# Performance work log

Hardware: AMD Instinct MI355X
Metric: run time of the kernel (lower is better)

The kernel has to match this reference:

```python
import jax, jax.numpy as jnp
import numpy as np

DIM = 128          # per-stream channels (init arg `dim`)
C = 2 * DIM        # fused channels
NH = 8             # num_heads
HD = C // NH       # head_dim = 32
K = 3              # kernel_size
DIL = (2, 3)       # dilation list
ND = len(DIL)
SCALE = HD ** -0.5


def setup_inputs() -> dict:
    key = jax.random.key(0)
    ks = jax.random.split(key, 4)
    B, H, W = 4, 80, 80
    rgb = jax.random.normal(ks[0], (B, DIM, H, W), jnp.float32)
    ir = jax.random.normal(ks[1], (B, DIM, H, W), jnp.float32)
    w_qkv = jax.random.normal(ks[2], (3 * C, C), jnp.float32) * (C ** -0.5)
    w_proj = jax.random.normal(ks[3], (C, C), jnp.float32) * (C ** -0.5)
    b_proj = jnp.zeros((C,), jnp.float32)
    return {"rgb": rgb, "ir": ir, "w_qkv": w_qkv, "w_proj": w_proj, "b_proj": b_proj}


def _unfold(x, k, d):
    # nn.Unfold(k, dilation=d, padding=d*(k-1)//2, stride=1) -> [B, c, k*k, H, W]
    B, c, H, W = x.shape
    p = d * (k - 1) // 2
    xp = jnp.pad(x, ((0, 0), (0, 0), (p, p), (p, p)))
    pats = [xp[:, :, i * d:i * d + H, j * d:j * d + W]
            for i in range(k) for j in range(k)]
    return jnp.stack(pats, axis=2)


def _dilate_attention(q, k, v, d):
    # q,k,v: [B, c, H, W] with c = C // ND; attention over k*k dilated neighborhood
    B, c, H, W = q.shape
    h = c // HD
    N = H * W
    qr = q.reshape(B, h, HD, N)                      # [B,h,hd,N]
    ku = _unfold(k, K, d).reshape(B, h, HD, K * K, N)  # [B,h,hd,K2,N]
    vu = _unfold(v, K, d).reshape(B, h, HD, K * K, N)
    attn = jnp.einsum('bhdn,bhdkn->bhnk', qr, ku) * SCALE   # [B,h,N,K2]
    attn = jax.nn.softmax(attn, axis=-1)
    out = jnp.einsum('bhnk,bhdkn->bnhd', attn, vu)          # head-major channels
    return out.reshape(B, H, W, c)


def reference(rgb, ir, w_qkv, w_proj, b_proj):
    y = jnp.concatenate([rgb, ir], axis=1)            # [B, C, H, W]
    B, Cc, H, W = y.shape
    # 1x1 conv qkv, then split channels as [3, num_dilation, C//num_dilation]
    qkv = jnp.einsum('bchw,oc->bohw', y, w_qkv).reshape(B, 3, ND, Cc // ND, H, W)
    outs = [_dilate_attention(qkv[:, 0, i], qkv[:, 1, i], qkv[:, 2, i], DIL[i])
            for i in range(ND)]
    x = jnp.concatenate(outs, axis=-1)                # [B, H, W, C], dilation-major
    x = x @ w_proj.T + b_proj                         # proj Linear(C, C)
    # residual: add rgb to first half of channels, ir to second half
    return x + y.transpose(0, 2, 3, 1)
```

## Files before the change

### kernel.cpp

```cpp
#include <hip/hip_runtime.h>

#define HH 80
#define WW 80
#define NPIX 6400
#define NB 4
#define BN 25600
#define CDIM 256
#define QKVC 768
#define SCALE 0.17677669529663689f

typedef __attribute__((ext_vector_type(8))) short short8;
typedef __attribute__((ext_vector_type(4))) float floatx4;

__device__ __forceinline__ float b2f(ushort u) {
    return __uint_as_float(((uint)u) << 16);
}
__device__ __forceinline__ ushort f2b(float f) {
    uint u = __float_as_uint(f);
    return (ushort)((u + 0x7fffu + ((u >> 16) & 1u)) >> 16);
}
__device__ __forceinline__ void unpack8(uint4 v, float* f) {
    f[0] = __uint_as_float(v.x << 16); f[1] = __uint_as_float(v.x & 0xffff0000u);
    f[2] = __uint_as_float(v.y << 16); f[3] = __uint_as_float(v.y & 0xffff0000u);
    f[4] = __uint_as_float(v.z << 16); f[5] = __uint_as_float(v.z & 0xffff0000u);
    f[6] = __uint_as_float(v.w << 16); f[7] = __uint_as_float(v.w & 0xffff0000u);
}
__device__ __forceinline__ void gload_lds16(const void* gptr, void* lptr) {
    __builtin_amdgcn_global_load_lds(
        (const __attribute__((address_space(1))) unsigned int*)gptr,
        (__attribute__((address_space(3))) unsigned int*)lptr,
        16, 0, 0);
}

__global__ __launch_bounds__(256) void cast_all_k(
    const float* __restrict__ rgb, const float* __restrict__ ir,
    const float* __restrict__ wq, const float* __restrict__ wp,
    ushort* __restrict__ Yb, ushort* __restrict__ wqb, ushort* __restrict__ wpb)
{
    const int tid = threadIdx.x;
    if (blockIdx.x >= 100) {
        int i = (((blockIdx.x - 100) * 8 + blockIdx.y) * 4 + blockIdx.z) * 256 + tid;
        if (i < QKVC * CDIM) wqb[i] = f2b(wq[i]);
        else                 wpb[i - QKVC * CDIM] = f2b(wp[i - QKVC * CDIM]);
        return;
    }
    __shared__ ushort T[32][72];
    const int pix0 = blockIdx.x * 64;
    const int cb = blockIdx.y;
    const int b = blockIdx.z;

    const int pl = tid & 63, cg = tid >> 6;
    #pragma unroll
    for (int cc = 0; cc < 32; cc += 4) {
        int c = cb * 32 + cc + cg;
        const float* src = (c < 128) ? (rgb + ((size_t)b * 128 + c) * NPIX)
                                     : (ir + ((size_t)b * 128 + (c - 128)) * NPIX);
        T[cc + cg][pl] = f2b(src[pix0 + pl]);
    }
    __syncthreads();
    const int nl = tid >> 2, c0 = (tid & 3) * 8;
    ushort tmp[8];
    #pragma unroll
    for (int j = 0; j < 8; ++j) tmp[j] = T[c0 + j][nl];
    uint4 v;
    v.x = tmp[0] | ((uint)tmp[1] << 16);
    v.y = tmp[2] | ((uint)tmp[3] << 16);
    v.z = tmp[4] | ((uint)tmp[5] << 16);
    v.w = tmp[6] | ((uint)tmp[7] << 16);
    *(uint4*)(&Yb[((size_t)(b * NPIX + pix0 + nl)) * CDIM + cb * 32 + c0]) = v;
}

__device__ __forceinline__ void gemm_nt_body64(
    const ushort* __restrict__ A, const ushort* __restrict__ W,
    ushort* As, ushort* Bs, int n0, int o0, floatx4 acc[4][4])
{
    const int tid = threadIdx.x;
    const int lane = tid & 63;
    const int wave = tid >> 6;
    const int wr = wave >> 1, wc = wave & 1;
    const int l15 = lane & 15, quad = lane >> 4;

    const int srow8 = tid >> 3;
    const int scol  = ((tid & 7) * 8) ^ ((srow8 & 1) << 5);
    const int par   = l15 & 1;

    for (int k0 = 0; k0 < CDIM; k0 += 64) {
        #pragma unroll
        for (int r = 0; r < 4; ++r) {
            const int row = r * 32 + srow8;
            gload_lds16(&A[(size_t)(n0 + row) * CDIM + k0 + scol],
                        As + r * 2048 + wave * 512);
            gload_lds16(&W[(size_t)(o0 + row) * CDIM + k0 + scol],
                        Bs + r * 2048 + wave * 512);
        }
        __syncthreads();
        #pragma unroll
        for (int s = 0; s < 2; ++s) {
            const int fc = ((s ^ par) << 5) + quad * 8;
            short8 af[4], bfr[4];
            #pragma unroll
            for (int i = 0; i < 4; ++i)
                af[i] = *(const short8*)(&As[(wr * 64 + i * 16 + l15) * 64 + fc]);
            #pragma unroll
            for (int j = 0; j < 4; ++j)
                bfr[j] = *(const short8*)(&Bs[(wc * 64 + j * 16 + l15) * 64 + fc]);
            #pragma unroll
            for (int i = 0; i < 4; ++i)
                #pragma unroll
                for (int j = 0; j < 4; ++j)
                    acc[i][j] = __builtin_amdgcn_mfma_f32_16x16x32_bf16(
                        bfr[j], af[i], acc[i][j], 0, 0, 0);
        }
        __syncthreads();
    }
}

__global__ __launch_bounds__(256) void gemm_qkv_mfma(
    const ushort* __restrict__ Yb, const ushort* __restrict__ Wb,
    ushort* __restrict__ qkv2)
{
    __shared__ __align__(16) ushort As[128 * 64];
    __shared__ __align__(16) ushort Bs[128 * 64];
    const int tid = threadIdx.x;
    const int lane = tid & 63;
    const int wave = tid >> 6;
    const int wr = wave >> 1, wc = wave & 1;
    const int l15 = lane & 15, quad = lane >> 4;

    const int bid = blockIdx.x;
    const int swz = (bid & 7) * 150 + (bid >> 3);
    const int n0 = (swz / 6) * 128;
    const int o0 = (swz % 6) * 128;

    floatx4 acc[4][4] = {};
    gemm_nt_body64(Yb, Wb, As, Bs, n0, o0, acc);

    #pragma unroll
    for (int i = 0; i < 4; ++i) {
        const int n = n0 + wr * 64 + i * 16 + l15;
        #pragma unroll
        for (int j = 0; j < 4; ++j) {
            const int o4 = o0 + wc * 64 + j * 16 + quad * 4;
            uint2 v;
            v.x = f2b(acc[i][j][0]) | ((uint)f2b(acc[i][j][1]) << 16);
            v.y = f2b(acc[i][j][2]) | ((uint)f2b(acc[i][j][3]) << 16);
            *(uint2*)(qkv2 + (size_t)(o4 >> 5) * BN * 32 + (size_t)n * 32 + (o4 & 31)) = v;
        }
    }
}

template<int D, bool EDGE>
__device__ __forceinline__ void attn_px(
    const ushort* __restrict__ qkv2, ushort* __restrict__ X2,
    int b, int dh, int y0, int x0)
{
    const int tid = threadIdx.x;
    const int px = tid & 15, py = tid >> 4;
    const int yy0 = y0 + py, xx0 = x0 + px;
    const int n = b * NPIX + yy0 * WW + xx0;
    const ushort* Qc = qkv2 + (size_t)dh * BN * 32;
    const ushort* Kc = qkv2 + (size_t)(8 + dh) * BN * 32;
    const ushort* Vc = qkv2 + (size_t)(16 + dh) * BN * 32;

    float q[32];
    {
        const uint4* qp = (const uint4*)(Qc + (size_t)n * 32);
        uint4 v0 = qp[0], v1 = qp[1], v2 = qp[2], v3 = qp[3];
        unpack8(v0, q); unpack8(v1, q + 8); unpack8(v2, q + 16); unpack8(v3, q + 24);
    }

    float sc[9];
    #pragma unroll
    for (int t = 0; t < 9; ++t) {
        const int dy = t / 3 - 1, dx = t % 3 - 1;
        int yy = yy0 + dy * D, xx = xx0 + dx * D;
        bool ok = true;
        if (EDGE) {
            ok = (yy >= 0 && yy < HH && xx >= 0 && xx < WW);
            yy = min(max(yy, 0), HH - 1);
            xx = min(max(xx, 0), WW - 1);
        }
        const uint4* kp = (const uint4*)(Kc + (size_t)(b * NPIX + yy * WW + xx) * 32);
        uint4 k0 = kp[0], k1 = kp[1], k2 = kp[2], k3 = kp[3];
        float kv[32];
        unpack8(k0, kv); unpack8(k1, kv + 8); unpack8(k2, kv + 16); unpack8(k3, kv + 24);
        float s = 0.f;
        #pragma unroll
        for (int j = 0; j < 32; ++j) s += q[j] * kv[j];
        sc[t] = (EDGE && !ok) ? 0.f : s * SCALE;
    }

    float m = sc[0];
    #pragma unroll
    for (int t = 1; t < 9; ++t) m = fmaxf(m, sc[t]);
    float sum = 0.f;
    #pragma unroll
    for (int t = 0; t < 9; ++t) { sc[t] = __expf(sc[t] - m); sum += sc[t]; }
    const float inv = 1.f / sum;

    float o[32];
    #pragma unroll
    for (int j = 0; j < 32; ++j) o[j] = 0.f;
    #pragma unroll
    for (int t = 0; t < 9; ++t) {
        const int dy = t / 3 - 1, dx = t % 3 - 1;
        int yy = yy0 + dy * D, xx = xx0 + dx * D;
        bool ok = true;
        if (EDGE) {
            ok = (yy >= 0 && yy < HH && xx >= 0 && xx < WW);
            yy = min(max(yy, 0), HH - 1);
            xx = min(max(xx, 0), WW - 1);
        }
        const uint4* vp = (const uint4*)(Vc + (size_t)(b * NPIX + yy * WW + xx) * 32);
        uint4 v0 = vp[0], v1 = vp[1], v2 = vp[2], v3 = vp[3];
        float vv[32];
        unpack8(v0, vv); unpack8(v1, vv + 8); unpack8(v2, vv + 16); unpack8(v3, vv + 24);
        const float wgt = (EDGE && !ok) ? 0.f : sc[t] * inv;
        #pragma unroll
        for (int j = 0; j < 32; ++j) o[j] += wgt * vv[j];
    }

    uint4* xp = (uint4*)(X2 + (size_t)dh * BN * 32 + (size_t)n * 32);
    #pragma unroll
    for (int m4 = 0; m4 < 4; ++m4) {
        uint4 v;
        v.x = f2b(o[8 * m4 + 0]) | ((uint)f2b(o[8 * m4 + 1]) << 16);
        v.y = f2b(o[8 * m4 + 2]) | ((uint)f2b(o[8 * m4 + 3]) << 16);
        v.z = f2b(o[8 * m4 + 4]) | ((uint)f2b(o[8 * m4 + 5]) << 16);
        v.w = f2b(o[8 * m4 + 6]) | ((uint)f2b(o[8 * m4 + 7]) << 16);
        xp[m4] = v;
    }
}

__global__ __launch_bounds__(256) void attn2_k(
    const ushort* __restrict__ qkv2, ushort* __restrict__ X2)
{
    const int bid = blockIdx.x;
    const int dh  = bid & 7;
    const int t2  = bid >> 3;
    const int b   = t2 / 25;
    const int tile = t2 % 25;
    const int y0 = (tile / 5) * 16, x0 = (tile % 5) * 16;
    const bool inter = (y0 >= 16 && y0 <= 48 && x0 >= 16 && x0 <= 48);
    if (dh < 4) {
        if (inter) attn_px<2, false>(qkv2, X2, b, dh, y0, x0);
        else       attn_px<2, true >(qkv2, X2, b, dh, y0, x0);
    } else {
        if (inter) attn_px<3, false>(qkv2, X2, b, dh, y0, x0);
        else       attn_px<3, true >(qkv2, X2, b, dh, y0, x0);
    }
}

__global__ __launch_bounds__(256) void proj_mfma(
    const ushort* __restrict__ X2, const ushort* __restrict__ Wpb,
    const float* __restrict__ bp, const ushort* __restrict__ Yb,
    float* __restrict__ out)
{
    __shared__ __align__(16) ushort As[64 * 64];
    __shared__ __align__(16) ushort Bs[128 * 64];
    const int tid = threadIdx.x;
    const int lane = tid & 63;
    const int wave = tid >> 6;
    const int wr = wave >> 1, wc = wave & 1;
    const int l15 = lane & 15, quad = lane >> 4;

    const int bid = blockIdx.x;
    const int swz = (bid & 7) * 100 + (bid >> 3);
    const int n0 = (swz >> 1) * 64;
    const int o0 = (swz & 1) * 128;

    const int srow8 = tid >> 3;
    const int scol  = ((tid & 7) * 8) ^ ((srow8 & 1) << 5);
    const int chunk_sel = ((tid >> 2) & 1) ^ (srow8 & 1);
    const int coff  = (tid & 3) * 8;
    const int par   = l15 & 1;

    floatx4 acc[2][4] = {};

    for (int k0 = 0; k0 < CDIM; k0 += 64) {
        const int cbase = k0 >> 5;
        const ushort* Achunk = X2 + (size_t)(cbase + chunk_sel) * BN * 32;
        #pragma unroll
        for (int r = 0; r < 2; ++r) {
            const int row = r * 32 + srow8;
            gload_lds16(&Achunk[(size_t)(n0 + row) * 32 + coff],
                        As + r * 2048 + wave * 512);
        }
        #pragma unroll
        for (int r = 0; r < 4; ++r) {
            const int row = r * 32 + srow8;
            gload_lds16(&Wpb[(size_t)(o0 + row) * CDIM + k0 + scol],
                        Bs + r * 2048 + wave * 512);
        }
        __syncthreads();
        #pragma unroll
        for (int s = 0; s < 2; ++s) {
            const int fc = ((s ^ par) << 5) + quad * 8;
            short8 af[2], bfr[4];
            #pragma unroll
            for (int i = 0; i < 2; ++i)
                af[i] = *(const short8*)(&As[(wr * 32 + i * 16 + l15) * 64 + fc]);
            #pragma unroll
            for (int j = 0; j < 4; ++j)
                bfr[j] = *(const short8*)(&Bs[(wc * 64 + j * 16 + l15) * 64 + fc]);
            #pragma unroll
            for (int i = 0; i < 2; ++i)
                #pragma unroll
                for (int j = 0; j < 4; ++j)
                    acc[i][j] = __builtin_amdgcn_mfma_f32_16x16x32_bf16(
                        bfr[j], af[i], acc[i][j], 0, 0, 0);
        }
        __syncthreads();
    }

    #pragma unroll
    for (int i = 0; i < 2; ++i) {
        const int n = n0 + wr * 32 + i * 16 + l15;
        #pragma unroll
        for (int j = 0; j < 4; ++j) {
            const int o4 = o0 + wc * 64 + j * 16 + quad * 4;
            const float4 bias = *(const float4*)(bp + o4);
            const ushort4 res = *(const ushort4*)(Yb + (size_t)n * CDIM + o4);
            float4 v;
            v.x = acc[i][j][0] + bias.x + b2f(res.x);
            v.y = acc[i][j][1] + bias.y + b2f(res.y);
            v.z = acc[i][j][2] + bias.z + b2f(res.z);
            v.w = acc[i][j][3] + bias.w + b2f(res.w);
            *(float4*)(out + (size_t)n * CDIM + o4) = v;
        }
    }
}

extern "C" void kernel_launch(void* const* d_in, const int* in_sizes, int n_in,
                              void* d_out, int out_size, void* d_ws, size_t ws_size,
                              hipStream_t stream) {
    const float* rgb    = (const float*)d_in[0];
    const float* ir     = (const float*)d_in[1];
    const float* w_qkv  = (const float*)d_in[2];
    const float* w_proj = (const float*)d_in[3];
    const float* b_proj = (const float*)d_in[4];
    float* out = (float*)d_out;

    ushort* qkv2 = (ushort*)d_ws;
    ushort* Yb   = qkv2 + (size_t)24 * BN * 32;
    ushort* X2   = Yb + (size_t)BN * CDIM;
    ushort* Wqb  = X2 + (size_t)8 * BN * 32;
    ushort* Wpb  = Wqb + (size_t)QKVC * CDIM;

    cast_all_k<<<dim3(132, 8, NB), 256, 0, stream>>>(rgb, ir, w_qkv, w_proj,
                                                     Yb, Wqb, Wpb);
    gemm_qkv_mfma<<<dim3(1200), 256, 0, stream>>>(Yb, Wqb, qkv2);
    attn2_k<<<dim3(800), 256, 0, stream>>>(qkv2, X2);
    proj_mfma<<<dim3(800), 256, 0, stream>>>(X2, Wpb, b_proj, Yb, out);
}
```

Before: 140.2 us.

## Fuse dilated attention into projection GEMM via shared-memory tile

The attention and output projection kernels are merged into one. Each block computes attention for an 8x4 pixel tile across all 8 heads and writes the bf16 result into a swizzled LDS buffer. It then runs the projection GEMM over all 256 output channels straight from LDS. This removes the X2 global round trip and one kernel launch. In exchange each block now reloads the full projection weight matrix and runs attention on only 32 pixels per head, with smaller spatial tiles for neighbour reuse.

```diff
diff --git a/kernel.cpp b/kernel.cpp
--- a/kernel.cpp
+++ b/kernel.cpp
@@ -150,13 +150,12 @@
 }
 
 template<int D, bool EDGE>
-__device__ __forceinline__ void attn_px(
-    const ushort* __restrict__ qkv2, ushort* __restrict__ X2,
-    int b, int dh, int y0, int x0)
-{
-    const int tid = threadIdx.x;
-    const int px = tid & 15, py = tid >> 4;
-    const int yy0 = y0 + py, xx0 = x0 + px;
+__device__ __forceinline__ void attn_phase(
+    const ushort* __restrict__ qkv2, ushort* Xl,
+    int b, int dh, int y0, int x0, int px)
+{
+    const int py = px >> 3, pxx = px & 7;
+    const int yy0 = y0 + py, xx0 = x0 + pxx;
     const int n = b * NPIX + yy0 * WW + xx0;
     const ushort* Qc = qkv2 + (size_t)dh * BN * 32;
     const ushort* Kc = qkv2 + (size_t)(8 + dh) * BN * 32;
@@ -220,7 +219,6 @@
         for (int j = 0; j < 32; ++j) o[j] += wgt * vv[j];
     }
 
-    uint4* xp = (uint4*)(X2 + (size_t)dh * BN * 32 + (size_t)n * 32);
     #pragma unroll
     for (int m4 = 0; m4 < 4; ++m4) {
         uint4 v;
@@ -228,68 +226,51 @@
         v.y = f2b(o[8 * m4 + 2]) | ((uint)f2b(o[8 * m4 + 3]) << 16);
         v.z = f2b(o[8 * m4 + 4]) | ((uint)f2b(o[8 * m4 + 5]) << 16);
         v.w = f2b(o[8 * m4 + 6]) | ((uint)f2b(o[8 * m4 + 7]) << 16);
-        xp[m4] = v;
-    }
-}
-
-__global__ __launch_bounds__(256) void attn2_k(
-    const ushort* __restrict__ qkv2, ushort* __restrict__ X2)
-{
-    const int bid = blockIdx.x;
-    const int dh  = bid & 7;
-    const int t2  = bid >> 3;
-    const int b   = t2 / 25;
-    const int tile = t2 % 25;
-    const int y0 = (tile / 5) * 16, x0 = (tile % 5) * 16;
-    const bool inter = (y0 >= 16 && y0 <= 48 && x0 >= 16 && x0 <= 48);
-    if (dh < 4) {
-        if (inter) attn_px<2, false>(qkv2, X2, b, dh, y0, x0);
-        else       attn_px<2, true >(qkv2, X2, b, dh, y0, x0);
-    } else {
-        if (inter) attn_px<3, false>(qkv2, X2, b, dh, y0, x0);
-        else       attn_px<3, true >(qkv2, X2, b, dh, y0, x0);
-    }
-}
-
-__global__ __launch_bounds__(256) void proj_mfma(
-    const ushort* __restrict__ X2, const ushort* __restrict__ Wpb,
+        const int slot = (dh * 4 + m4) ^ (px & 7);
+        *(uint4*)(&Xl[px * 256 + slot * 8]) = v;
+    }
+}
+
+__global__ __launch_bounds__(256) void attn_proj_k(
+    const ushort* __restrict__ qkv2, const ushort* __restrict__ Wpb,
     const float* __restrict__ bp, const ushort* __restrict__ Yb,
     float* __restrict__ out)
 {
-    __shared__ __align__(16) ushort As[64 * 64];
-    __shared__ __align__(16) ushort Bs[128 * 64];
+    __shared__ __align__(16) ushort Xl[32 * 256];
+    __shared__ __align__(16) ushort Bs[256 * 64];
     const int tid = threadIdx.x;
+    const int bid = blockIdx.x;
+    const int swz = (bid & 7) * 100 + (bid >> 3);
+    const int b  = swz / 200;
+    const int t  = swz % 200;
+    const int y0 = (t / 10) * 4, x0 = (t % 10) * 8;
+    const bool inter = (y0 >= 4 && y0 <= 72 && x0 >= 8 && x0 <= 64);
+
+    const int px = tid & 31;
+    const int dh = tid >> 5;
+
+    if (dh < 4) {
+        if (inter) attn_phase<2, false>(qkv2, Xl, b, dh, y0, x0, px);
+        else       attn_phase<2, true >(qkv2, Xl, b, dh, y0, x0, px);
+    } else {
+        if (inter) attn_phase<3, false>(qkv2, Xl, b, dh, y0, x0, px);
+        else       attn_phase<3, true >(qkv2, Xl, b, dh, y0, x0, px);
+    }
+    __syncthreads();
+
     const int lane = tid & 63;
     const int wave = tid >> 6;
-    const int wr = wave >> 1, wc = wave & 1;
     const int l15 = lane & 15, quad = lane >> 4;
-
-    const int bid = blockIdx.x;
-    const int swz = (bid & 7) * 100 + (bid >> 3);
-    const int n0 = (swz >> 1) * 64;
-    const int o0 = (swz & 1) * 128;
-
     const int srow8 = tid >> 3;
     const int scol  = ((tid & 7) * 8) ^ ((srow8 & 1) << 5);
-    const int chunk_sel = ((tid >> 2) & 1) ^ (srow8 & 1);
-    const int coff  = (tid & 3) * 8;
     const int par   = l15 & 1;
 
     floatx4 acc[2][4] = {};
-
     for (int k0 = 0; k0 < CDIM; k0 += 64) {
-        const int cbase = k0 >> 5;
-        const ushort* Achunk = X2 + (size_t)(cbase + chunk_sel) * BN * 32;
-        #pragma unroll
-        for (int r = 0; r < 2; ++r) {
+        #pragma unroll
+        for (int r = 0; r < 8; ++r) {
             const int row = r * 32 + srow8;
-            gload_lds16(&Achunk[(size_t)(n0 + row) * 32 + coff],
-                        As + r * 2048 + wave * 512);
-        }
-        #pragma unroll
-        for (int r = 0; r < 4; ++r) {
-            const int row = r * 32 + srow8;
-            gload_lds16(&Wpb[(size_t)(o0 + row) * CDIM + k0 + scol],
+            gload_lds16(&Wpb[(size_t)row * CDIM + k0 + scol],
                         Bs + r * 2048 + wave * 512);
         }
         __syncthreads();
@@ -298,11 +279,14 @@
             const int fc = ((s ^ par) << 5) + quad * 8;
             short8 af[2], bfr[4];
             #pragma unroll
-            for (int i = 0; i < 2; ++i)
-                af[i] = *(const short8*)(&As[(wr * 32 + i * 16 + l15) * 64 + fc]);
+            for (int i = 0; i < 2; ++i) {
+                const int row = i * 16 + l15;
+                const int slot = ((k0 >> 3) + s * 4 + quad) ^ (row & 7);
+                af[i] = *(const short8*)(&Xl[row * 256 + slot * 8]);
+            }
             #pragma unroll
             for (int j = 0; j < 4; ++j)
-                bfr[j] = *(const short8*)(&Bs[(wc * 64 + j * 16 + l15) * 64 + fc]);
+                bfr[j] = *(const short8*)(&Bs[(wave * 64 + j * 16 + l15) * 64 + fc]);
             #pragma unroll
             for (int i = 0; i < 2; ++i)
                 #pragma unroll
@@ -315,10 +299,11 @@
 
     #pragma unroll
     for (int i = 0; i < 2; ++i) {
-        const int n = n0 + wr * 32 + i * 16 + l15;
+        const int r15 = i * 16 + l15;
+        const int n = b * NPIX + (y0 + (r15 >> 3)) * WW + (x0 + (r15 & 7));
         #pragma unroll
         for (int j = 0; j < 4; ++j) {
-            const int o4 = o0 + wc * 64 + j * 16 + quad * 4;
+            const int o4 = wave * 64 + j * 16 + quad * 4;
             const float4 bias = *(const float4*)(bp + o4);
             const ushort4 res = *(const ushort4*)(Yb + (size_t)n * CDIM + o4);
             float4 v;
@@ -343,13 +328,11 @@
 
     ushort* qkv2 = (ushort*)d_ws;
     ushort* Yb   = qkv2 + (size_t)24 * BN * 32;
-    ushort* X2   = Yb + (size_t)BN * CDIM;
-    ushort* Wqb  = X2 + (size_t)8 * BN * 32;
+    ushort* Wqb  = Yb + (size_t)BN * CDIM;
     ushort* Wpb  = Wqb + (size_t)QKVC * CDIM;
 
     cast_all_k<<<dim3(132, 8, NB), 256, 0, stream>>>(rgb, ir, w_qkv, w_proj,
                                                      Yb, Wqb, Wpb);
     gemm_qkv_mfma<<<dim3(1200), 256, 0, stream>>>(Yb, Wqb, qkv2);
-    attn2_k<<<dim3(800), 256, 0, stream>>>(qkv2, X2);
-    proj_mfma<<<dim3(800), 256, 0, stream>>>(X2, Wpb, b_proj, Yb, out);
-}
+    attn_proj_k<<<dim3(800), 256, 0, stream>>>(qkv2, Wpb, b_proj, Yb, out);
+}
```

After: 137.9 us. Within noise of the previous version (-1.6%).
